# Performance work log

Hardware: AMD Instinct MI355X
Metric: run time of the kernel (lower is better)

The kernel has to match this reference:

```python
import jax, jax.numpy as jnp
import numpy as np

B, L, D, H = 2, 2048, 1024, 16
DK = D // H


def setup_inputs() -> dict:
    key = jax.random.key(0)
    ks = jax.random.split(key, 12)
    s = 1.0 / np.sqrt(D)
    return {
        "x": jax.random.normal(ks[0], (B, L, D), jnp.float32),
        "timestamps": jnp.sort(jax.random.uniform(ks[1], (B, L), jnp.float32) * 1000.0, axis=-1),
        "decay_values": jax.random.normal(ks[2], (B, L), jnp.float32),
        "pad_mask": jnp.ones((B, L), dtype=bool),
        "Wq": jax.random.normal(ks[3], (D, D), jnp.float32) * s,
        "bq": jnp.zeros((D,), jnp.float32),
        "Wk": jax.random.normal(ks[4], (D, D), jnp.float32) * s,
        "bk": jnp.zeros((D,), jnp.float32),
        "Wv": jax.random.normal(ks[5], (D, D), jnp.float32) * s,
        "bv": jnp.zeros((D,), jnp.float32),
        "Wo": jax.random.normal(ks[6], (D, D), jnp.float32) * s,
        "bo": jnp.zeros((D,), jnp.float32),
        "lam": jnp.float32(0.01),
    }


def reference(x, timestamps, decay_values, pad_mask, Wq, bq, Wk, bk, Wv, bv, Wo, bo, lam):
    b, l, d = x.shape
    # projections (torch Linear: x @ W.T + b), split heads -> [B,H,L,DK]
    def split_heads(y):
        return y.reshape(b, l, H, DK).transpose(0, 2, 1, 3)
    Q = split_heads(x @ Wq.T + bq)
    K = split_heads(x @ Wk.T + bk)
    V = split_heads(x @ Wv.T + bv)

    scores = jnp.einsum("bhqd,bhkd->bhqk", Q, K) / np.sqrt(DK)
    # temporal log-decay bias
    t_diff = jnp.abs(timestamps[:, :, None] - timestamps[:, None, :])  # [B,L,L]
    denom = jax.lax.stop_gradient(jnp.maximum(t_diff.max(), 1.0))  # matches .item() constant
    scores = scores - jnp.abs(lam) * jnp.log1p(t_diff / denom)[:, None, :, :]

    causal = jnp.triu(jnp.ones((l, l), dtype=bool), k=1)  # True above diag -> masked
    neg_inf = jnp.float32(-jnp.inf)
    scores = jnp.where(causal[None, None], neg_inf, scores)
    scores = jnp.where(pad_mask[:, None, None, :], scores, neg_inf)

    attn = jnp.nan_to_num(jax.nn.softmax(scores, axis=-1), nan=0.0)
    out = jnp.einsum("bhqk,bhkd->bhqd", attn, V)
    out = out.transpose(0, 2, 1, 3).reshape(b, l, d)
    return out @ Wo.T + bo
```

## Files before the change

### kernel.cpp

```cpp
#include <hip/hip_runtime.h>
#include <hip/hip_bf16.h>
#include <math.h>

#define Bsz 2
#define Lsz 2048
#define Dsz 1024
#define Hsz 16
#define DKsz 64
#define NW_ELEMS (1u << 20)

typedef __attribute__((ext_vector_type(8))) short short8;
typedef __attribute__((ext_vector_type(4))) float v4f;
typedef unsigned short ushortT;
#define MFMA16(a, b, c) __builtin_amdgcn_mfma_f32_16x16x32_bf16(a, b, c, 0, 0, 0)
#define LOG2E 1.44269504088896340736f

__device__ __forceinline__ ushortT f2bf(float f) {
    union { float f; unsigned u; } x; x.f = f;
    unsigned r = x.u + 0x7fffu + ((x.u >> 16) & 1u);
    return (ushortT)(r >> 16);
}
__device__ __forceinline__ void glds16(const void* g, void* l) {
    __builtin_amdgcn_global_load_lds(
        (const __attribute__((address_space(1))) void*)g,
        (__attribute__((address_space(3))) void*)l, 16, 0, 0);
}

__global__ __launch_bounds__(256) void cast_denom(const float* __restrict__ x,
                                                  const float* __restrict__ Wq,
                                                  const float* __restrict__ Wk,
                                                  const float* __restrict__ Wv,
                                                  const float* __restrict__ Wo,
                                                  const float* __restrict__ t,
                                                  const float* __restrict__ bq,
                                                  const float* __restrict__ bk,
                                                  const float* __restrict__ bv,
                                                  ushortT* __restrict__ xb,
                                                  ushortT* __restrict__ Wqkvb,
                                                  ushortT* __restrict__ Wob,
                                                  float* __restrict__ denom_out,
                                                  float* __restrict__ cbias,
                                                  int ncast) {
    const int NX = Bsz * Lsz * Dsz;
    int tid = threadIdx.x;
    if ((int)blockIdx.x == ncast) {
        __shared__ float smx[256], smn[256];
        for (int i = tid; i < 3 * Dsz; i += 256)
            cbias[i] = (i < Dsz) ? bq[i] : (i < 2 * Dsz ? bk[i - Dsz] : bv[i - 2 * Dsz]);
        float best = 1.0f;
        for (int b = 0; b < Bsz; ++b) {
            float mx = -INFINITY, mn = INFINITY;
            for (int i = tid; i < Lsz; i += 256) {
                float v = t[b * Lsz + i];
                mx = fmaxf(mx, v);
                mn = fminf(mn, v);
            }
            smx[tid] = mx; smn[tid] = mn;
            __syncthreads();
            for (int s = 128; s > 0; s >>= 1) {
                if (tid < s) {
                    smx[tid] = fmaxf(smx[tid], smx[tid + s]);
                    smn[tid] = fminf(smn[tid], smn[tid + s]);
                }
                __syncthreads();
            }
            best = fmaxf(best, smx[0] - smn[0]);
            __syncthreads();
        }
        if (tid == 0) denom_out[0] = best;
        return;
    }
    int i = (blockIdx.x * 256 + tid) * 4;
    const float* src; ushortT* dst;
    if (i < NX) { src = x + i; dst = xb + i; }
    else {
        int j = i - NX;
        if (j < 3 * (int)NW_ELEMS) {
            int w = j >> 20, o = j & (NW_ELEMS - 1);
            src = (w == 0 ? Wq : (w == 1 ? Wk : Wv)) + o;
            dst = Wqkvb + j;
        } else {
            int o = j - 3 * NW_ELEMS;
            src = Wo + o; dst = Wob + o;
        }
    }
    float4 v = *(const float4*)src;
    ushort4 o4;
    o4.x = f2bf(v.x); o4.y = f2bf(v.y); o4.z = f2bf(v.z); o4.w = f2bf(v.w);
    *(ushort4*)dst = o4;
}

template <bool QKV, int MT>
__global__ __launch_bounds__(256) void gemm_mfma(const ushortT* __restrict__ A,
                                                 const ushortT* __restrict__ W,
                                                 const float* __restrict__ bias,
                                                 void* __restrict__ O0,
                                                 void* __restrict__ O1,
                                                 void* __restrict__ O2) {
    const int K = Dsz;
    constexpr int NTI = (MT == 128) ? 4 : 2;
    __shared__ ushortT As[2 * MT * 32];
    __shared__ ushortT Ws[2 * 128 * 32];
    int tid = threadIdx.x;
    int wid = tid >> 6, lane = tid & 63, quad = lane >> 4, m16 = lane & 15;
    int wm = (MT == 128) ? (wid >> 1) : 0;
    int wn = (MT == 128) ? (wid & 1) : wid;
    int m0 = blockIdx.y * MT, n0 = blockIdx.x * 128;
    int lrow = lane >> 2, lcol = (lane & 3) * 8;

    v4f acc[4][NTI];
#pragma unroll
    for (int i = 0; i < 4; ++i)
#pragma unroll
        for (int j = 0; j < NTI; ++j) acc[i][j] = (v4f){0.f, 0.f, 0.f, 0.f};

    for (int kt = 0; kt < K; kt += 64) {
        __syncthreads();
#pragma unroll
        for (int p = 0; p < 2; ++p) {
            int kp = kt + p * 32 + lcol;
            if (MT == 128) {
#pragma unroll
                for (int hf = 0; hf < 2; ++hf) {
                    int r0 = wid * 32 + hf * 16;
                    glds16(A + (size_t)(m0 + r0 + lrow) * K + kp,
                           &As[p * MT * 32 + r0 * 32]);
                }
            } else {
                int r0 = wid * 16;
                glds16(A + (size_t)(m0 + r0 + lrow) * K + kp,
                       &As[p * MT * 32 + r0 * 32]);
            }
#pragma unroll
            for (int hf = 0; hf < 2; ++hf) {
                int r0 = wid * 32 + hf * 16;
                glds16(W + (size_t)(n0 + r0 + lrow) * K + kp,
                       &Ws[p * 128 * 32 + r0 * 32]);
            }
        }
        __syncthreads();
#pragma unroll
        for (int p = 0; p < 2; ++p) {
            short8 af[4], wf[NTI];
#pragma unroll
            for (int mt = 0; mt < 4; ++mt)
                af[mt] = *(const short8*)&As[p * MT * 32 +
                                            (wm * 64 + mt * 16 + m16) * 32 + quad * 8];
#pragma unroll
            for (int nt = 0; nt < NTI; ++nt)
                wf[nt] = *(const short8*)&Ws[p * 128 * 32 +
                                            (wn * 16 * NTI + nt * 16 + m16) * 32 + quad * 8];
#pragma unroll
            for (int mt = 0; mt < 4; ++mt)
#pragma unroll
                for (int nt = 0; nt < NTI; ++nt)
                    acc[mt][nt] = MFMA16(af[mt], wf[nt], acc[mt][nt]);
        }
    }

    if (QKV) {
        int region = n0 >> 10;
        float scale = (region == 0) ? 0.125f * LOG2E : 1.0f;
#pragma unroll
        for (int nt = 0; nt < NTI; ++nt) {
            int col = n0 + wn * 16 * NTI + nt * 16 + m16;
            float bv_ = bias[col];
            int c1 = col & (Dsz - 1);
#pragma unroll
            for (int mt = 0; mt < 4; ++mt) {
                int row0 = m0 + wm * 64 + mt * 16 + quad * 4;
                if (region == 2) {
                    ushort4 pk;
                    pk.x = f2bf(acc[mt][nt][0] + bv_);
                    pk.y = f2bf(acc[mt][nt][1] + bv_);
                    pk.z = f2bf(acc[mt][nt][2] + bv_);
                    pk.w = f2bf(acc[mt][nt][3] + bv_);
                    int bb = row0 >> 11, seq = row0 & (Lsz - 1);
                    *(ushort4*)&((ushortT*)O2)[((size_t)bb * Dsz + c1) * Lsz + seq] = pk;
                } else {
                    ushortT* dst = (ushortT*)(region == 0 ? O0 : O1);
#pragma unroll
                    for (int r = 0; r < 4; ++r)
                        dst[(size_t)(row0 + r) * Dsz + c1] =
                            f2bf((acc[mt][nt][r] + bv_) * scale);
                }
            }
        }
    } else {
#pragma unroll
        for (int nt = 0; nt < NTI; ++nt) {
            int col = n0 + wn * 16 * NTI + nt * 16 + m16;
            float bv_ = bias[col];
#pragma unroll
            for (int mt = 0; mt < 4; ++mt) {
                int row0 = m0 + wm * 64 + mt * 16 + quad * 4;
#pragma unroll
                for (int r = 0; r < 4; ++r)
                    ((float*)O0)[(size_t)(row0 + r) * Dsz + col] = acc[mt][nt][r] + bv_;
            }
        }
    }
}

__global__ __launch_bounds__(256) void attn_mfma(const ushortT* __restrict__ Qb,
                                                 const ushortT* __restrict__ Kb,
                                                 const ushortT* __restrict__ Vtg,
                                                 const float* __restrict__ ts,
                                                 const float* __restrict__ denomp,
                                                 const float* __restrict__ lamp,
                                                 ushortT* __restrict__ AOb) {
    int id = blockIdx.x;
    int xcd = id & 7, cu = (id >> 3) & 31, j = id >> 8;
    int bh = xcd * 4 + (cu >> 3);
    int b = bh >> 4, h = bh & 15;
    int p = ((cu & 7) << 1) | (j >> 1);
    int qt = (j & 1) ? (31 - p) : p;

    int tid = threadIdx.x;
    int wid = tid >> 6, lane = tid & 63, quad = lane >> 4, m16 = lane & 15;

    __shared__ ushortT Ks[64 * 72];
    __shared__ ushortT Vs[64 * 72];
    __shared__ ushortT Pl[4][16 * 72];
    __shared__ float tks[64];

    float denom = denomp[0];
    float alam = fabsf(lamp[0]);
    const size_t bL = (size_t)b * Lsz;

    int sr = tid >> 2, sc = (tid & 3) * 16;

    int q0 = qt * 64;
    int ntiles = qt + 1;

    int qrow = q0 + wid * 16 + m16;
    const ushortT* qptr = Qb + (bL + qrow) * Dsz + h * 64 + quad * 8;
    short8 qf0 = *(const short8*)qptr;
    short8 qf1 = *(const short8*)(qptr + 32);

    float tq[4];
    int gq[4];
#pragma unroll
    for (int r = 0; r < 4; ++r) {
        gq[r] = q0 + wid * 16 + quad * 4 + r;
        tq[r] = ts[bL + gq[r]];
    }

    v4f o[4];
    float lacc[4];
#pragma unroll
    for (int i = 0; i < 4; ++i) { o[i] = (v4f){0.f, 0.f, 0.f, 0.f}; lacc[i] = 0.f; }

    uint4 kv0, kv1, vv0, vv1;
    float tkv = 0.f;
    {
        const ushortT* ksrc = Kb + (bL + sr) * Dsz + h * 64 + sc;
        const ushortT* vsrc = Vtg + ((size_t)b * Dsz + h * 64 + sr) * Lsz + sc;
        kv0 = *(const uint4*)ksrc; kv1 = *(const uint4*)(ksrc + 8);
        vv0 = *(const uint4*)vsrc; vv1 = *(const uint4*)(vsrc + 8);
        if (tid < 64) tkv = ts[bL + tid];
    }

    for (int jt = 0; jt < ntiles; ++jt) {
        int k0 = jt * 64;
        __syncthreads();
        *(uint4*)&Ks[sr * 72 + sc] = kv0; *(uint4*)&Ks[sr * 72 + sc + 8] = kv1;
        *(uint4*)&Vs[sr * 72 + sc] = vv0; *(uint4*)&Vs[sr * 72 + sc + 8] = vv1;
        if (tid < 64) tks[tid] = tkv;
        __syncthreads();
        if (jt + 1 < ntiles) {
            int k1 = k0 + 64;
            const ushortT* ksrc = Kb + (bL + k1 + sr) * Dsz + h * 64 + sc;
            const ushortT* vsrc = Vtg + ((size_t)b * Dsz + h * 64 + sr) * Lsz + k1 + sc;
            kv0 = *(const uint4*)ksrc; kv1 = *(const uint4*)(ksrc + 8);
            vv0 = *(const uint4*)vsrc; vv1 = *(const uint4*)(vsrc + 8);
            if (tid < 64) tkv = ts[bL + k1 + tid];
        }

        v4f s[4];
#pragma unroll
        for (int ct = 0; ct < 4; ++ct) {
            short8 kf0 = *(const short8*)&Ks[(ct * 16 + m16) * 72 + quad * 8];
            short8 kf1 = *(const short8*)&Ks[(ct * 16 + m16) * 72 + 32 + quad * 8];
            s[ct] = (v4f){0.f, 0.f, 0.f, 0.f};
            s[ct] = MFMA16(qf0, kf0, s[ct]);
            s[ct] = MFMA16(qf1, kf1, s[ct]);
        }

        bool diag = (jt == qt);
#pragma unroll
        for (int ct = 0; ct < 4; ++ct) {
            int gk = k0 + ct * 16 + m16;
            float tk = tks[ct * 16 + m16];
#pragma unroll
            for (int r = 0; r < 4; ++r) {
                float w = denom + (tq[r] - tk);
                float f = fmaf(-alam, __builtin_amdgcn_logf(w), s[ct][r]);
                if (diag) f = (gk <= gq[r]) ? f : -INFINITY;
                float pv = __builtin_amdgcn_exp2f(f);
                unsigned pu = __builtin_bit_cast(unsigned, pv);
                Pl[wid][(quad * 4 + r) * 72 + ct * 16 + m16] = (ushortT)(pu >> 16);
                lacc[r] += __builtin_bit_cast(float, pu & 0xffff0000u);
            }
        }

        short8 pf0 = *(const short8*)&Pl[wid][m16 * 72 + quad * 8];
        short8 pf1 = *(const short8*)&Pl[wid][m16 * 72 + 32 + quad * 8];
#pragma unroll
        for (int dt = 0; dt < 4; ++dt) {
            short8 vf0 = *(const short8*)&Vs[(dt * 16 + m16) * 72 + quad * 8];
            short8 vf1 = *(const short8*)&Vs[(dt * 16 + m16) * 72 + 32 + quad * 8];
            o[dt] = MFMA16(pf0, vf0, o[dt]);
            o[dt] = MFMA16(pf1, vf1, o[dt]);
        }
    }

#pragma unroll
    for (int r = 0; r < 4; ++r) {
        float l = lacc[r];
#pragma unroll
        for (int off = 1; off < 16; off <<= 1)
            l += __shfl_xor(l, off, 16);
        float invl = 1.0f / l;
#pragma unroll
        for (int dt = 0; dt < 4; ++dt) {
            int col = h * 64 + dt * 16 + m16;
            AOb[(bL + gq[r]) * Dsz + col] = f2bf(o[dt][r] * invl);
        }
    }
}

extern "C" void kernel_launch(void* const* d_in, const int* in_sizes, int n_in,
                              void* d_out, int out_size, void* d_ws, size_t ws_size,
                              hipStream_t stream) {
    const float* x   = (const float*)d_in[0];
    const float* ts  = (const float*)d_in[1];
    const float* Wq  = (const float*)d_in[4];
    const float* bq  = (const float*)d_in[5];
    const float* Wk  = (const float*)d_in[6];
    const float* bk  = (const float*)d_in[7];
    const float* Wv  = (const float*)d_in[8];
    const float* bv  = (const float*)d_in[9];
    const float* Wo  = (const float*)d_in[10];
    const float* bo  = (const float*)d_in[11];
    const float* lam = (const float*)d_in[12];

    const size_t NX = (size_t)Bsz * Lsz * Dsz;
    const size_t NW = (size_t)NW_ELEMS;

    char* w = (char*)d_ws;
    float* denom = (float*)w;            w += 256;
    float* cbias = (float*)w;            w += 3 * Dsz * 4 + 256;
    ushortT* xb    = (ushortT*)w;        w += NX * 2;
    ushortT* Wqkvb = (ushortT*)w;        w += 3 * NW * 2;
    ushortT* Wob   = (ushortT*)w;        w += NW * 2;
    ushortT* Qb    = (ushortT*)w;        w += NX * 2;
    ushortT* Kbf   = (ushortT*)w;        w += NX * 2;
    ushortT* Vtg   = (ushortT*)w;        w += NX * 2;
    ushortT* AOb   = (ushortT*)w;        w += NX * 2;

    int ncast = (int)((NX + 4 * NW) / 4 / 256);
    cast_denom<<<ncast + 1, 256, 0, stream>>>(x, Wq, Wk, Wv, Wo, ts, bq, bk, bv,
                                              xb, Wqkvb, Wob, denom, cbias, ncast);

    dim3 gqkv(3 * Dsz / 128, (Bsz * Lsz) / 128);
    gemm_mfma<true, 128><<<gqkv, 256, 0, stream>>>(xb, Wqkvb, cbias, Qb, Kbf, Vtg);

    attn_mfma<<<1024, 256, 0, stream>>>(Qb, Kbf, Vtg, ts, denom, lam, AOb);

    dim3 gout(Dsz / 128, (Bsz * Lsz) / 64);
    gemm_mfma<false, 64><<<gout, 256, 0, stream>>>(AOb, Wob, bo, d_out, nullptr, nullptr);
}
```

Before: 218.8 us.

## Generalize GEMM tiling and remap blocks so each XCD owns a weight column slice

```diff
diff --git a/kernel.cpp b/kernel.cpp
--- a/kernel.cpp
+++ b/kernel.cpp
@@ -90,7 +90,7 @@
     *(ushort4*)dst = o4;
 }
 
-template <bool QKV, int MT>
+template <bool QKV, int MT, int NT, int WMW, int WNW, int PERX>
 __global__ __launch_bounds__(256) void gemm_mfma(const ushortT* __restrict__ A,
                                                  const ushortT* __restrict__ W,
                                                  const float* __restrict__ bias,
@@ -98,19 +98,22 @@
                                                  void* __restrict__ O1,
                                                  void* __restrict__ O2) {
     const int K = Dsz;
-    constexpr int NTI = (MT == 128) ? 4 : 2;
+    constexpr int MROWS = MT / WMW, NCOLS = NT / WNW;
+    constexpr int MTI = MROWS / 16, NTI = NCOLS / 16;
     __shared__ ushortT As[2 * MT * 32];
-    __shared__ ushortT Ws[2 * 128 * 32];
+    __shared__ ushortT Ws[2 * NT * 32];
     int tid = threadIdx.x;
     int wid = tid >> 6, lane = tid & 63, quad = lane >> 4, m16 = lane & 15;
-    int wm = (MT == 128) ? (wid >> 1) : 0;
-    int wn = (MT == 128) ? (wid & 1) : wid;
-    int m0 = blockIdx.y * MT, n0 = blockIdx.x * 128;
+    int wm = wid / WNW, wn = wid % WNW;
+    int id = blockIdx.x;
+    int xcd = id & 7, r = id >> 3;
+    int n0 = (xcd * PERX + r % PERX) * NT;
+    int m0 = (r / PERX) * MT;
     int lrow = lane >> 2, lcol = (lane & 3) * 8;
 
-    v4f acc[4][NTI];
-#pragma unroll
-    for (int i = 0; i < 4; ++i)
+    v4f acc[MTI][NTI];
+#pragma unroll
+    for (int i = 0; i < MTI; ++i)
 #pragma unroll
         for (int j = 0; j < NTI; ++j) acc[i][j] = (v4f){0.f, 0.f, 0.f, 0.f};
 
@@ -119,39 +122,31 @@
 #pragma unroll
         for (int p = 0; p < 2; ++p) {
             int kp = kt + p * 32 + lcol;
-            if (MT == 128) {
-#pragma unroll
-                for (int hf = 0; hf < 2; ++hf) {
-                    int r0 = wid * 32 + hf * 16;
-                    glds16(A + (size_t)(m0 + r0 + lrow) * K + kp,
-                           &As[p * MT * 32 + r0 * 32]);
-                }
-            } else {
-                int r0 = wid * 16;
-                glds16(A + (size_t)(m0 + r0 + lrow) * K + kp,
-                       &As[p * MT * 32 + r0 * 32]);
-            }
-#pragma unroll
-            for (int hf = 0; hf < 2; ++hf) {
-                int r0 = wid * 32 + hf * 16;
-                glds16(W + (size_t)(n0 + r0 + lrow) * K + kp,
-                       &Ws[p * 128 * 32 + r0 * 32]);
+#pragma unroll
+            for (int i = 0; i < MT / 64; ++i) {
+                int r0 = wid * (MT / 4) + i * 16;
+                glds16(A + (size_t)(m0 + r0 + lrow) * K + kp, &As[p * MT * 32 + r0 * 32]);
+            }
+#pragma unroll
+            for (int i = 0; i < NT / 64; ++i) {
+                int r0 = wid * (NT / 4) + i * 16;
+                glds16(W + (size_t)(n0 + r0 + lrow) * K + kp, &Ws[p * NT * 32 + r0 * 32]);
             }
         }
         __syncthreads();
 #pragma unroll
         for (int p = 0; p < 2; ++p) {
-            short8 af[4], wf[NTI];
-#pragma unroll
-            for (int mt = 0; mt < 4; ++mt)
+            short8 af[MTI], wf[NTI];
+#pragma unroll
+            for (int mt = 0; mt < MTI; ++mt)
                 af[mt] = *(const short8*)&As[p * MT * 32 +
-                                            (wm * 64 + mt * 16 + m16) * 32 + quad * 8];
+                                            (wm * MROWS + mt * 16 + m16) * 32 + quad * 8];
 #pragma unroll
             for (int nt = 0; nt < NTI; ++nt)
-                wf[nt] = *(const short8*)&Ws[p * 128 * 32 +
-                                            (wn * 16 * NTI + nt * 16 + m16) * 32 + quad * 8];
-#pragma unroll
-            for (int mt = 0; mt < 4; ++mt)
+                wf[nt] = *(const short8*)&Ws[p * NT * 32 +
+                                            (wn * NCOLS + nt * 16 + m16) * 32 + quad * 8];
+#pragma unroll
+            for (int mt = 0; mt < MTI; ++mt)
 #pragma unroll
                 for (int nt = 0; nt < NTI; ++nt)
                     acc[mt][nt] = MFMA16(af[mt], wf[nt], acc[mt][nt]);
@@ -163,12 +158,12 @@
         float scale = (region == 0) ? 0.125f * LOG2E : 1.0f;
 #pragma unroll
         for (int nt = 0; nt < NTI; ++nt) {
-            int col = n0 + wn * 16 * NTI + nt * 16 + m16;
+            int col = n0 + wn * NCOLS + nt * 16 + m16;
             float bv_ = bias[col];
             int c1 = col & (Dsz - 1);
 #pragma unroll
-            for (int mt = 0; mt < 4; ++mt) {
-                int row0 = m0 + wm * 64 + mt * 16 + quad * 4;
+            for (int mt = 0; mt < MTI; ++mt) {
+                int row0 = m0 + wm * MROWS + mt * 16 + quad * 4;
                 if (region == 2) {
                     ushort4 pk;
                     pk.x = f2bf(acc[mt][nt][0] + bv_);
@@ -180,23 +175,23 @@
                 } else {
                     ushortT* dst = (ushortT*)(region == 0 ? O0 : O1);
 #pragma unroll
-                    for (int r = 0; r < 4; ++r)
-                        dst[(size_t)(row0 + r) * Dsz + c1] =
-                            f2bf((acc[mt][nt][r] + bv_) * scale);
+                    for (int rr = 0; rr < 4; ++rr)
+                        dst[(size_t)(row0 + rr) * Dsz + c1] =
+                            f2bf((acc[mt][nt][rr] + bv_) * scale);
                 }
             }
         }
     } else {
 #pragma unroll
         for (int nt = 0; nt < NTI; ++nt) {
-            int col = n0 + wn * 16 * NTI + nt * 16 + m16;
+            int col = n0 + wn * NCOLS + nt * 16 + m16;
             float bv_ = bias[col];
 #pragma unroll
-            for (int mt = 0; mt < 4; ++mt) {
-                int row0 = m0 + wm * 64 + mt * 16 + quad * 4;
-#pragma unroll
-                for (int r = 0; r < 4; ++r)
-                    ((float*)O0)[(size_t)(row0 + r) * Dsz + col] = acc[mt][nt][r] + bv_;
+            for (int mt = 0; mt < MTI; ++mt) {
+                int row0 = m0 + wm * MROWS + mt * 16 + quad * 4;
+#pragma unroll
+                for (int rr = 0; rr < 4; ++rr)
+                    ((float*)O0)[(size_t)(row0 + rr) * Dsz + col] = acc[mt][nt][rr] + bv_;
             }
         }
     }
@@ -363,11 +358,11 @@
     cast_denom<<<ncast + 1, 256, 0, stream>>>(x, Wq, Wk, Wv, Wo, ts, bq, bk, bv,
                                               xb, Wqkvb, Wob, denom, cbias, ncast);
 
-    dim3 gqkv(3 * Dsz / 128, (Bsz * Lsz) / 128);
-    gemm_mfma<true, 128><<<gqkv, 256, 0, stream>>>(xb, Wqkvb, cbias, Qb, Kbf, Vtg);
+    gemm_mfma<true, 64, 128, 1, 4, 3><<<1536, 256, 0, stream>>>(
+        xb, Wqkvb, cbias, Qb, Kbf, Vtg);
 
     attn_mfma<<<1024, 256, 0, stream>>>(Qb, Kbf, Vtg, ts, denom, lam, AOb);
 
-    dim3 gout(Dsz / 128, (Bsz * Lsz) / 64);
-    gemm_mfma<false, 64><<<gout, 256, 0, stream>>>(AOb, Wob, bo, d_out, nullptr, nullptr);
-}
+    gemm_mfma<false, 64, 64, 2, 2, 2><<<1024, 256, 0, stream>>>(
+        AOb, Wob, bo, d_out, nullptr, nullptr);
+}
```

Measured after the change: 214.2 us. 1.02x faster.
